# Kernel tuning notes

Measured on AMD Instinct MI355X. Metric: run time of the kernel, lower is better.

Reference implementation:

```python
import jax, jax.numpy as jnp
import numpy as np
from jax import lax

PS = 8  # patch size

def setup_inputs() -> dict:
    key = jax.random.key(0)
    ks = jax.random.split(key, 7)
    dim = 64
    B, H, W = 4, 256, 256
    x = jax.random.normal(ks[0], (B, dim, H, W), dtype=jnp.float32)
    # to_hidden: Conv2d(dim, 6*dim, k=1)
    w_hidden = jax.random.normal(ks[1], (6 * dim, dim, 1, 1), dtype=jnp.float32) * 0.05
    b_hidden = jax.random.normal(ks[2], (6 * dim,), dtype=jnp.float32) * 0.01
    # to_hidden_dw: depthwise Conv2d(6*dim, 6*dim, k=3, pad=1, groups=6*dim)
    w_dw = jax.random.normal(ks[3], (6 * dim, 1, 3, 3), dtype=jnp.float32) * 0.05
    b_dw = jax.random.normal(ks[4], (6 * dim,), dtype=jnp.float32) * 0.01
    # project_out: Conv2d(2*dim, dim, k=1)
    w_out = jax.random.normal(ks[5], (dim, 2 * dim, 1, 1), dtype=jnp.float32) * 0.05
    b_out = jax.random.normal(ks[6], (dim,), dtype=jnp.float32) * 0.01
    return {"x": x, "w_hidden": w_hidden, "b_hidden": b_hidden,
            "w_dw": w_dw, "b_dw": b_dw, "w_out": w_out, "b_out": b_out}

def _conv(x, w, groups=1, padding='VALID'):
    return lax.conv_general_dilated(
        x, w, window_strides=(1, 1), padding=padding,
        dimension_numbers=('NCHW', 'OIHW', 'NCHW'),
        feature_group_count=groups)

def reference(x, w_hidden, b_hidden, w_dw, b_dw, w_out, b_out):
    # 1x1 expansion to 6*dim channels
    hidden = _conv(x, w_hidden) + b_hidden[None, :, None, None]
    # 3x3 depthwise conv (groups == channels)
    dw = _conv(hidden, w_dw, groups=w_dw.shape[0], padding='SAME') + b_dw[None, :, None, None]
    q, k, v = jnp.split(dw, 3, axis=1)  # each (B, 2*dim, H, W)
    B, C, H, W = q.shape
    # raw reshape into (B,C,H/8,W/8,8,8) exactly as torch .reshape on contiguous NCHW
    q_patch = q.reshape(B, C, H // PS, W // PS, PS, PS)
    k_patch = k.reshape(B, C, H // PS, W // PS, PS, PS)
    q_fft = jnp.fft.rfft2(q_patch)
    k_fft = jnp.fft.rfft2(k_patch)
    out = jnp.fft.irfft2(q_fft * k_fft, s=(PS, PS))  # circular conv of q,k patches
    out = out.reshape(B, C, (H // PS) * PS, (W // PS) * PS)
    output = v * out
    output = _conv(output, w_out) + b_out[None, :, None, None]
    return output
```

## Files before the change

### kernel.cpp

```cpp
#include <hip/hip_runtime.h>

#define HW 65536
#define W_IMG 256
#define H_IMG 256
#define CIN 64
#define CHID 384
#define CQK 128

__global__ __launch_bounds__(256) void k1_expand(
    const float* __restrict__ x_base,
    const float* __restrict__ wh,
    const float* __restrict__ bh,
    float* __restrict__ hidden_base,
    size_t x_bstride, size_t hid_bstride)
{
    const float* x = x_base + blockIdx.z * x_bstride;
    float* hidden  = hidden_base + blockIdx.z * hid_bstride;
    const int pxbase = blockIdx.x * 256;
    const int cobase = blockIdx.y * 48;
    const int tid  = threadIdx.x;
    const int lane = tid & 63;
    const int wq   = __builtin_amdgcn_readfirstlane(tid >> 6);
    const int px   = pxbase + lane * 4;

    #pragma unroll
    for (int g = 0; g < 2; ++g) {
        const int cw = cobase + g * 24 + wq * 6;
        float acc[6][4];
        #pragma unroll
        for (int i = 0; i < 6; ++i)
            #pragma unroll
            for (int j = 0; j < 4; ++j) acc[i][j] = 0.f;

        float4 xa[4], xb[4];
        #pragma unroll
        for (int u = 0; u < 4; ++u)
            xa[u] = *reinterpret_cast<const float4*>(&x[(size_t)u * HW + px]);

        #pragma unroll 1
        for (int ci4 = 0; ci4 < CIN; ci4 += 8) {
            #pragma unroll
            for (int u = 0; u < 4; ++u)
                xb[u] = *reinterpret_cast<const float4*>(&x[(size_t)(ci4 + 4 + u) * HW + px]);
            #pragma unroll
            for (int i = 0; i < 6; ++i) {
                float4 wv = *reinterpret_cast<const float4*>(
                    &wh[(size_t)(cw + i) * CIN + ci4]);
                float wu[4] = {wv.x, wv.y, wv.z, wv.w};
                #pragma unroll
                for (int u = 0; u < 4; ++u) {
                    acc[i][0] += wu[u] * xa[u].x;
                    acc[i][1] += wu[u] * xa[u].y;
                    acc[i][2] += wu[u] * xa[u].z;
                    acc[i][3] += wu[u] * xa[u].w;
                }
            }
            if (ci4 + 8 < CIN) {
                #pragma unroll
                for (int u = 0; u < 4; ++u)
                    xa[u] = *reinterpret_cast<const float4*>(&x[(size_t)(ci4 + 8 + u) * HW + px]);
            }
            #pragma unroll
            for (int i = 0; i < 6; ++i) {
                float4 wv = *reinterpret_cast<const float4*>(
                    &wh[(size_t)(cw + i) * CIN + ci4 + 4]);
                float wu[4] = {wv.x, wv.y, wv.z, wv.w};
                #pragma unroll
                for (int u = 0; u < 4; ++u) {
                    acc[i][0] += wu[u] * xb[u].x;
                    acc[i][1] += wu[u] * xb[u].y;
                    acc[i][2] += wu[u] * xb[u].z;
                    acc[i][3] += wu[u] * xb[u].w;
                }
            }
        }

        #pragma unroll
        for (int i = 0; i < 6; ++i) {
            int co = cw + i;
            float b = bh[co];
            float4 o;
            o.x = acc[i][0] + b; o.y = acc[i][1] + b;
            o.z = acc[i][2] + b; o.w = acc[i][3] + b;
            *reinterpret_cast<float4*>(&hidden[(size_t)co * HW + px]) = o;
        }
    }
}

#define QK_CH   2208
#define QK_ROW  276
#define QK_SEG  68
__global__ __launch_bounds__(256) void k2_fused(
    const float* __restrict__ hidden_base,
    const float* __restrict__ wdw,
    const float* __restrict__ bdw,
    float* __restrict__ vout_base,
    size_t hid_bstride, size_t vout_bstride)
{
    __shared__ float qk[2 * QK_CH];

    const float* hidden = hidden_base + blockIdx.z * hid_bstride;
    float* vout         = vout_base + blockIdx.z * vout_bstride;

    const int c  = blockIdx.y;
    const int r0 = blockIdx.x * 8;
    const int tid = threadIdx.x;

    const int row   = tid >> 5;
    const int col32 = tid & 31;
    const int px8   = col32 * 8;
    const int gro   = r0 + row;

    float4 qa0[3], qa1[3], ka0[3], ka1[3];
    #pragma unroll
    for (int ky = 0; ky < 3; ++ky) {
        int grr = gro + ky - 1;
        qa0[ky] = make_float4(0.f,0.f,0.f,0.f); qa1[ky] = qa0[ky];
        ka0[ky] = qa0[ky];                      ka1[ky] = qa0[ky];
        if ((unsigned)grr < H_IMG) {
            const float* rq = hidden + (size_t)c * HW + (size_t)grr * W_IMG;
            const float* rk = hidden + (size_t)(c + CQK) * HW + (size_t)grr * W_IMG;
            qa0[ky] = *reinterpret_cast<const float4*>(&rq[px8]);
            qa1[ky] = *reinterpret_cast<const float4*>(&rq[px8 + 4]);
            ka0[ky] = *reinterpret_cast<const float4*>(&rk[px8]);
            ka1[ky] = *reinterpret_cast<const float4*>(&rk[px8 + 4]);
        }
    }

    #pragma unroll
    for (int ch = 0; ch < 2; ++ch) {
        const float4* a0 = ch ? ka0 : qa0;
        const float4* a1 = ch ? ka1 : qa1;
        const float* wv = wdw + (c + ch * CQK) * 9;
        const float bias = bdw[c + ch * CQK];

        float accd[8];
        #pragma unroll
        for (int j = 0; j < 8; ++j) accd[j] = bias;

        #pragma unroll
        for (int ky = 0; ky < 3; ++ky) {
            float kw0 = wv[ky * 3], kw1 = wv[ky * 3 + 1], kw2 = wv[ky * 3 + 2];
            float lf = __shfl_up(a1[ky].w, 1);
            float rt = __shfl_down(a0[ky].x, 1);
            if (col32 == 0)  lf = 0.f;
            if (col32 == 31) rt = 0.f;
            float h[10] = {lf, a0[ky].x, a0[ky].y, a0[ky].z, a0[ky].w,
                               a1[ky].x, a1[ky].y, a1[ky].z, a1[ky].w, rt};
            #pragma unroll
            for (int j = 0; j < 8; ++j)
                accd[j] += h[j] * kw0 + h[j + 1] * kw1 + h[j + 2] * kw2;
        }

        float* dst = &qk[ch * QK_CH + row * QK_ROW + (px8 >> 6) * QK_SEG + (px8 & 63)];
        float4 o0, o1;
        o0.x = accd[0]; o0.y = accd[1]; o0.z = accd[2]; o0.w = accd[3];
        o1.x = accd[4]; o1.y = accd[5]; o1.z = accd[6]; o1.w = accd[7];
        *reinterpret_cast<float4*>(dst)     = o0;
        *reinterpret_cast<float4*>(dst + 4) = o1;
    }

    const int seg = (tid >> 3) & 3;
    const int i   = tid & 7;
    const int gr  = r0 + row;
    const int wp0 = seg * 64 + i * 8;

    const float* hbv = hidden + (size_t)(c + 2 * CQK) * HW;
    float4 hv[3][2];
    float  hm[3], hp[3];
    #pragma unroll
    for (int ky = 0; ky < 3; ++ky) {
        int grr = gr + ky - 1;
        hv[ky][0] = make_float4(0.f,0.f,0.f,0.f);
        hv[ky][1] = make_float4(0.f,0.f,0.f,0.f);
        hm[ky] = 0.f; hp[ky] = 0.f;
        if ((unsigned)grr < H_IMG) {
            const float* rb = hbv + (size_t)grr * W_IMG;
            hv[ky][0] = *reinterpret_cast<const float4*>(&rb[wp0]);
            hv[ky][1] = *reinterpret_cast<const float4*>(&rb[wp0 + 4]);
            hm[ky] = (wp0 > 0)   ? rb[wp0 - 1] : 0.f;
            hp[ky] = (wp0 < 248) ? rb[wp0 + 8] : 0.f;
        }
    }

    __syncthreads();

    const float* qb = &qk[row * QK_ROW + seg * QK_SEG];
    const float* kb = &qk[QK_CH + row * QK_ROW + seg * QK_SEG];

    float acc[8];
    #pragma unroll
    for (int j = 0; j < 8; ++j) acc[j] = 0.f;

    #pragma unroll
    for (int s = 0; s < 8; ++s) {
        int qr = (i - s) & 7;
        float4 ka = *reinterpret_cast<const float4*>(&kb[s * 8]);
        float4 kc = *reinterpret_cast<const float4*>(&kb[s * 8 + 4]);
        float4 qa = *reinterpret_cast<const float4*>(&qb[qr * 8]);
        float4 qc = *reinterpret_cast<const float4*>(&qb[qr * 8 + 4]);
        float kr[8] = {ka.x, ka.y, ka.z, ka.w, kc.x, kc.y, kc.z, kc.w};
        float qv[8] = {qa.x, qa.y, qa.z, qa.w, qc.x, qc.y, qc.z, qc.w};
        #pragma unroll
        for (int t = 0; t < 8; ++t)
            #pragma unroll
            for (int j = 0; j < 8; ++j)
                acc[j] += kr[t] * qv[(j - t) & 7];
    }

    const float* wvv = wdw + (c + 2 * CQK) * 9;
    const float vbias = bdw[c + 2 * CQK];
    float vc[8];
    #pragma unroll
    for (int j = 0; j < 8; ++j) vc[j] = vbias;
    #pragma unroll
    for (int ky = 0; ky < 3; ++ky) {
        float kw0 = wvv[ky * 3], kw1 = wvv[ky * 3 + 1], kw2 = wvv[ky * 3 + 2];
        float h[10];
        h[0] = hm[ky];
        h[1] = hv[ky][0].x; h[2] = hv[ky][0].y; h[3] = hv[ky][0].z; h[4] = hv[ky][0].w;
        h[5] = hv[ky][1].x; h[6] = hv[ky][1].y; h[7] = hv[ky][1].z; h[8] = hv[ky][1].w;
        h[9] = hp[ky];
        #pragma unroll
        for (int j = 0; j < 8; ++j)
            vc[j] += h[j] * kw0 + h[j + 1] * kw1 + h[j + 2] * kw2;
    }

    float* dst = &vout[(size_t)c * HW + (size_t)gr * W_IMG + wp0];
    float4 o0, o1;
    o0.x = acc[0] * vc[0]; o0.y = acc[1] * vc[1];
    o0.z = acc[2] * vc[2]; o0.w = acc[3] * vc[3];
    o1.x = acc[4] * vc[4]; o1.y = acc[5] * vc[5];
    o1.z = acc[6] * vc[6]; o1.w = acc[7] * vc[7];
    *reinterpret_cast<float4*>(dst)     = o0;
    *reinterpret_cast<float4*>(dst + 4) = o1;
}

__global__ __launch_bounds__(256) void k3_project(
    const float* __restrict__ vout_base,
    const float* __restrict__ wo,
    const float* __restrict__ bo,
    float* __restrict__ out_base,
    size_t vout_bstride, size_t out_bstride)
{
    const float* vout = vout_base + blockIdx.z * vout_bstride;
    float* out        = out_base + blockIdx.z * out_bstride;
    const int pxbase = blockIdx.x * 256;
    const int cobase = blockIdx.y * 16;
    const int tid  = threadIdx.x;
    const int lane = tid & 63;
    const int wq   = __builtin_amdgcn_readfirstlane(tid >> 6);
    const int px   = pxbase + lane * 4;
    const int cw   = cobase + wq * 4;

    float acc[4][4];
    #pragma unroll
    for (int i = 0; i < 4; ++i)
        #pragma unroll
        for (int j = 0; j < 4; ++j) acc[i][j] = 0.f;

    float4 xa[4], xb[4];
    #pragma unroll
    for (int u = 0; u < 4; ++u)
        xa[u] = *reinterpret_cast<const float4*>(&vout[(size_t)u * HW + px]);

    #pragma unroll 1
    for (int cc4 = 0; cc4 < CQK; cc4 += 8) {
        #pragma unroll
        for (int u = 0; u < 4; ++u)
            xb[u] = *reinterpret_cast<const float4*>(&vout[(size_t)(cc4 + 4 + u) * HW + px]);
        #pragma unroll
        for (int i = 0; i < 4; ++i) {
            float4 wv = *reinterpret_cast<const float4*>(
                &wo[(size_t)(cw + i) * CQK + cc4]);
            float wu[4] = {wv.x, wv.y, wv.z, wv.w};
            #pragma unroll
            for (int u = 0; u < 4; ++u) {
                acc[i][0] += wu[u] * xa[u].x;
                acc[i][1] += wu[u] * xa[u].y;
                acc[i][2] += wu[u] * xa[u].z;
                acc[i][3] += wu[u] * xa[u].w;
            }
        }
        if (cc4 + 8 < CQK) {
            #pragma unroll
            for (int u = 0; u < 4; ++u)
                xa[u] = *reinterpret_cast<const float4*>(&vout[(size_t)(cc4 + 8 + u) * HW + px]);
        }
        #pragma unroll
        for (int i = 0; i < 4; ++i) {
            float4 wv = *reinterpret_cast<const float4*>(
                &wo[(size_t)(cw + i) * CQK + cc4 + 4]);
            float wu[4] = {wv.x, wv.y, wv.z, wv.w};
            #pragma unroll
            for (int u = 0; u < 4; ++u) {
                acc[i][0] += wu[u] * xb[u].x;
                acc[i][1] += wu[u] * xb[u].y;
                acc[i][2] += wu[u] * xb[u].z;
                acc[i][3] += wu[u] * xb[u].w;
            }
        }
    }

    #pragma unroll
    for (int i = 0; i < 4; ++i) {
        int co = cw + i;
        float b = bo[co];
        float4 o;
        o.x = acc[i][0] + b; o.y = acc[i][1] + b;
        o.z = acc[i][2] + b; o.w = acc[i][3] + b;
        *reinterpret_cast<float4*>(&out[(size_t)co * HW + px]) = o;
    }
}

extern "C" void kernel_launch(void* const* d_in, const int* in_sizes, int n_in,
                              void* d_out, int out_size, void* d_ws, size_t ws_size,
                              hipStream_t stream) {
    const float* x   = (const float*)d_in[0];
    const float* wh  = (const float*)d_in[1];
    const float* bh  = (const float*)d_in[2];
    const float* wdw = (const float*)d_in[3];
    const float* bdw = (const float*)d_in[4];
    const float* wo  = (const float*)d_in[5];
    const float* bo  = (const float*)d_in[6];
    float* out = (float*)d_out;

    const size_t n_hid  = (size_t)CHID * HW;
    const size_t n_vout = (size_t)CQK * HW;
    const size_t n_x    = (size_t)CIN * HW;

    if (ws_size >= 4 * (n_hid + n_vout) * sizeof(float)) {
        float* hidden = (float*)d_ws;
        float* vout   = hidden + 4 * n_hid;
        k1_expand <<<dim3(HW / 256, CHID / 48, 4), 256, 0, stream>>>(
            x, wh, bh, hidden, n_x, n_hid);
        k2_fused  <<<dim3(H_IMG / 8, CQK, 4),      256, 0, stream>>>(
            hidden, wdw, bdw, vout, n_hid, n_vout);
        k3_project<<<dim3(HW / 256, 64 / 16, 4),   256, 0, stream>>>(
            vout, wo, bo, out, n_vout, n_x);
    } else {
        float* hidden = (float*)d_ws;
        float* vout   = hidden + n_hid;
        for (int b = 0; b < 4; ++b) {
            const float* xb = x + (size_t)b * n_x;
            float* ob       = out + (size_t)b * n_x;
            k1_expand <<<dim3(HW / 256, CHID / 48, 1), 256, 0, stream>>>(
                xb, wh, bh, hidden, 0, 0);
            k2_fused  <<<dim3(H_IMG / 8, CQK, 1),      256, 0, stream>>>(
                hidden, wdw, bdw, vout, 0, 0);
            k3_project<<<dim3(HW / 256, 64 / 16, 1),   256, 0, stream>>>(
                vout, wo, bo, ob, 0, 0);
        }
    }
}
```

Before: 424.8 us.

## Widen k1 channel tile with triple-buffered loads; enlarge k2 row tile

After: 942.5 us. 122% more time.

```diff
diff --git a/kernel.cpp b/kernel.cpp
--- a/kernel.cpp
+++ b/kernel.cpp
@@ -6,6 +6,19 @@
 #define CIN 64
 #define CHID 384
 #define CQK 128
+
+#define K1_LOAD(B, CHUNK) { \
+    _Pragma("unroll") for (int u = 0; u < 4; ++u) \
+        B[u] = *reinterpret_cast<const float4*>(&x[(size_t)((CHUNK) * 4 + u) * HW + px]); }
+#define K1_COMP(B, CHUNK) { \
+    _Pragma("unroll") for (int i = 0; i < 12; ++i) { \
+        float4 wv = *reinterpret_cast<const float4*>(&wh[(size_t)(cw + i) * CIN + (CHUNK) * 4]); \
+        float wu[4] = {wv.x, wv.y, wv.z, wv.w}; \
+        _Pragma("unroll") for (int u = 0; u < 4; ++u) { \
+            acc[i][0] += wu[u] * B[u].x; \
+            acc[i][1] += wu[u] * B[u].y; \
+            acc[i][2] += wu[u] * B[u].z; \
+            acc[i][3] += wu[u] * B[u].w; } } }
 
 __global__ __launch_bounds__(256) void k1_expand(
     const float* __restrict__ x_base,
@@ -22,74 +35,75 @@
     const int lane = tid & 63;
     const int wq   = __builtin_amdgcn_readfirstlane(tid >> 6);
     const int px   = pxbase + lane * 4;
-
-    #pragma unroll
-    for (int g = 0; g < 2; ++g) {
-        const int cw = cobase + g * 24 + wq * 6;
-        float acc[6][4];
-        #pragma unroll
-        for (int i = 0; i < 6; ++i)
-            #pragma unroll
-            for (int j = 0; j < 4; ++j) acc[i][j] = 0.f;
-
-        float4 xa[4], xb[4];
-        #pragma unroll
-        for (int u = 0; u < 4; ++u)
-            xa[u] = *reinterpret_cast<const float4*>(&x[(size_t)u * HW + px]);
-
-        #pragma unroll 1
-        for (int ci4 = 0; ci4 < CIN; ci4 += 8) {
-            #pragma unroll
-            for (int u = 0; u < 4; ++u)
-                xb[u] = *reinterpret_cast<const float4*>(&x[(size_t)(ci4 + 4 + u) * HW + px]);
-            #pragma unroll
-            for (int i = 0; i < 6; ++i) {
-                float4 wv = *reinterpret_cast<const float4*>(
-                    &wh[(size_t)(cw + i) * CIN + ci4]);
-                float wu[4] = {wv.x, wv.y, wv.z, wv.w};
+    const int cw   = cobase + wq * 12;
+
+    float acc[12][4];
+    #pragma unroll
+    for (int i = 0; i < 12; ++i)
+        #pragma unroll
+        for (int j = 0; j < 4; ++j) acc[i][j] = 0.f;
+
+    float4 b0[4], b1[4], b2[4];
+    K1_LOAD(b0, 0)
+    K1_LOAD(b1, 1)
+
+    #pragma unroll
+    for (int t = 0; t < 16; ++t) {
+        if (t + 2 < 16) {
+            if (((t + 2) % 3) == 0)      { K1_LOAD(b0, t + 2) }
+            else if (((t + 2) % 3) == 1) { K1_LOAD(b1, t + 2) }
+            else                         { K1_LOAD(b2, t + 2) }
+        }
+        if ((t % 3) == 0)      { K1_COMP(b0, t) }
+        else if ((t % 3) == 1) { K1_COMP(b1, t) }
+        else                   { K1_COMP(b2, t) }
+    }
+
+    #pragma unroll
+    for (int i = 0; i < 12; ++i) {
+        int co = cw + i;
+        float b = bh[co];
+        float4 o;
+        o.x = acc[i][0] + b; o.y = acc[i][1] + b;
+        o.z = acc[i][2] + b; o.w = acc[i][3] + b;
+        *reinterpret_cast<float4*>(&hidden[(size_t)co * HW + px]) = o;
+    }
+}
+
+#define K2ROWS 32
+#define K2_CH  8704
+#define K2_ROW 272
+
+template<int I0>
+__device__ __forceinline__ void conv_half(
+    const float* __restrict__ qb, const float* __restrict__ kb, float acc[4][8])
+{
+    float qv[64];
+    #pragma unroll
+    for (int m = 0; m < 16; ++m) {
+        float4 t = *reinterpret_cast<const float4*>(&qb[m * 4]);
+        qv[m * 4]     = t.x;
+        qv[m * 4 + 1] = t.y;
+        qv[m * 4 + 2] = t.z;
+        qv[m * 4 + 3] = t.w;
+    }
+    #pragma unroll
+    for (int s = 0; s < 8; ++s) {
+        float4 ka = *reinterpret_cast<const float4*>(&kb[s * 8]);
+        float4 kc = *reinterpret_cast<const float4*>(&kb[s * 8 + 4]);
+        float kr[8] = {ka.x, ka.y, ka.z, ka.w, kc.x, kc.y, kc.z, kc.w};
+        #pragma unroll
+        for (int ii = 0; ii < 4; ++ii) {
+            const int qr = (I0 + ii - s) & 7;
+            #pragma unroll
+            for (int t = 0; t < 8; ++t)
                 #pragma unroll
-                for (int u = 0; u < 4; ++u) {
-                    acc[i][0] += wu[u] * xa[u].x;
-                    acc[i][1] += wu[u] * xa[u].y;
-                    acc[i][2] += wu[u] * xa[u].z;
-                    acc[i][3] += wu[u] * xa[u].w;
-                }
-            }
-            if (ci4 + 8 < CIN) {
-                #pragma unroll
-                for (int u = 0; u < 4; ++u)
-                    xa[u] = *reinterpret_cast<const float4*>(&x[(size_t)(ci4 + 8 + u) * HW + px]);
-            }
-            #pragma unroll
-            for (int i = 0; i < 6; ++i) {
-                float4 wv = *reinterpret_cast<const float4*>(
-                    &wh[(size_t)(cw + i) * CIN + ci4 + 4]);
-                float wu[4] = {wv.x, wv.y, wv.z, wv.w};
-                #pragma unroll
-                for (int u = 0; u < 4; ++u) {
-                    acc[i][0] += wu[u] * xb[u].x;
-                    acc[i][1] += wu[u] * xb[u].y;
-                    acc[i][2] += wu[u] * xb[u].z;
-                    acc[i][3] += wu[u] * xb[u].w;
-                }
-            }
-        }
-
-        #pragma unroll
-        for (int i = 0; i < 6; ++i) {
-            int co = cw + i;
-            float b = bh[co];
-            float4 o;
-            o.x = acc[i][0] + b; o.y = acc[i][1] + b;
-            o.z = acc[i][2] + b; o.w = acc[i][3] + b;
-            *reinterpret_cast<float4*>(&hidden[(size_t)co * HW + px]) = o;
-        }
-    }
-}
-
-#define QK_CH   2208
-#define QK_ROW  276
-#define QK_SEG  68
+                for (int j = 0; j < 8; ++j)
+                    acc[ii][j] += kr[t] * qv[qr * 8 + ((j - t) & 7)];
+        }
+    }
+}
+
 __global__ __launch_bounds__(256) void k2_fused(
     const float* __restrict__ hidden_base,
     const float* __restrict__ wdw,
@@ -97,143 +111,148 @@
     float* __restrict__ vout_base,
     size_t hid_bstride, size_t vout_bstride)
 {
-    __shared__ float qk[2 * QK_CH];
+    __shared__ float qk[2 * K2_CH];
 
     const float* hidden = hidden_base + blockIdx.z * hid_bstride;
     float* vout         = vout_base + blockIdx.z * vout_bstride;
 
     const int c  = blockIdx.y;
-    const int r0 = blockIdx.x * 8;
+    const int r0 = blockIdx.x * K2ROWS;
     const int tid = threadIdx.x;
 
-    const int row   = tid >> 5;
-    const int col32 = tid & 31;
-    const int px8   = col32 * 8;
-    const int gro   = r0 + row;
-
-    float4 qa0[3], qa1[3], ka0[3], ka1[3];
-    #pragma unroll
-    for (int ky = 0; ky < 3; ++ky) {
-        int grr = gro + ky - 1;
-        qa0[ky] = make_float4(0.f,0.f,0.f,0.f); qa1[ky] = qa0[ky];
-        ka0[ky] = qa0[ky];                      ka1[ky] = qa0[ky];
-        if ((unsigned)grr < H_IMG) {
-            const float* rq = hidden + (size_t)c * HW + (size_t)grr * W_IMG;
-            const float* rk = hidden + (size_t)(c + CQK) * HW + (size_t)grr * W_IMG;
-            qa0[ky] = *reinterpret_cast<const float4*>(&rq[px8]);
-            qa1[ky] = *reinterpret_cast<const float4*>(&rq[px8 + 4]);
-            ka0[ky] = *reinterpret_cast<const float4*>(&rk[px8]);
-            ka1[ky] = *reinterpret_cast<const float4*>(&rk[px8 + 4]);
-        }
-    }
-
-    #pragma unroll
-    for (int ch = 0; ch < 2; ++ch) {
-        const float4* a0 = ch ? ka0 : qa0;
-        const float4* a1 = ch ? ka1 : qa1;
-        const float* wv = wdw + (c + ch * CQK) * 9;
-        const float bias = bdw[c + ch * CQK];
-
-        float accd[8];
-        #pragma unroll
-        for (int j = 0; j < 8; ++j) accd[j] = bias;
-
-        #pragma unroll
-        for (int ky = 0; ky < 3; ++ky) {
-            float kw0 = wv[ky * 3], kw1 = wv[ky * 3 + 1], kw2 = wv[ky * 3 + 2];
-            float lf = __shfl_up(a1[ky].w, 1);
-            float rt = __shfl_down(a0[ky].x, 1);
-            if (col32 == 0)  lf = 0.f;
-            if (col32 == 31) rt = 0.f;
-            float h[10] = {lf, a0[ky].x, a0[ky].y, a0[ky].z, a0[ky].w,
-                               a1[ky].x, a1[ky].y, a1[ky].z, a1[ky].w, rt};
-            #pragma unroll
-            for (int j = 0; j < 8; ++j)
-                accd[j] += h[j] * kw0 + h[j + 1] * kw1 + h[j + 2] * kw2;
-        }
-
-        float* dst = &qk[ch * QK_CH + row * QK_ROW + (px8 >> 6) * QK_SEG + (px8 & 63)];
-        float4 o0, o1;
-        o0.x = accd[0]; o0.y = accd[1]; o0.z = accd[2]; o0.w = accd[3];
-        o1.x = accd[4]; o1.y = accd[5]; o1.z = accd[6]; o1.w = accd[7];
-        *reinterpret_cast<float4*>(dst)     = o0;
-        *reinterpret_cast<float4*>(dst + 4) = o1;
-    }
-
-    const int seg = (tid >> 3) & 3;
-    const int i   = tid & 7;
-    const int gr  = r0 + row;
-    const int wp0 = seg * 64 + i * 8;
-
-    const float* hbv = hidden + (size_t)(c + 2 * CQK) * HW;
-    float4 hv[3][2];
+    {
+        const int rowb  = tid >> 5;
+        const int col32 = tid & 31;
+        const int px8   = col32 * 8;
+        const float* wq9 = wdw + c * 9;
+        const float* wk9 = wdw + (c + CQK) * 9;
+        const float qb9 = bdw[c];
+        const float kb9 = bdw[c + CQK];
+
+        #pragma unroll
+        for (int rp = 0; rp < 4; ++rp) {
+            const int row_local = rp * 8 + rowb;
+            const int gro = r0 + row_local;
+
+            float4 qa0[3], qa1[3], ka0[3], ka1[3];
+            #pragma unroll
+            for (int ky = 0; ky < 3; ++ky) {
+                int grr = gro + ky - 1;
+                qa0[ky] = make_float4(0.f,0.f,0.f,0.f); qa1[ky] = qa0[ky];
+                ka0[ky] = qa0[ky];                      ka1[ky] = qa0[ky];
+                if ((unsigned)grr < H_IMG) {
+                    const float* rq = hidden + (size_t)c * HW + (size_t)grr * W_IMG;
+                    const float* rk = hidden + (size_t)(c + CQK) * HW + (size_t)grr * W_IMG;
+                    qa0[ky] = *reinterpret_cast<const float4*>(&rq[px8]);
+                    qa1[ky] = *reinterpret_cast<const float4*>(&rq[px8 + 4]);
+                    ka0[ky] = *reinterpret_cast<const float4*>(&rk[px8]);
+                    ka1[ky] = *reinterpret_cast<const float4*>(&rk[px8 + 4]);
+                }
+            }
+            #pragma unroll
+            for (int ch = 0; ch < 2; ++ch) {
+                const float4* a0 = ch ? ka0 : qa0;
+                const float4* a1 = ch ? ka1 : qa1;
+                const float* wv = ch ? wk9 : wq9;
+                float accd[8];
+                #pragma unroll
+                for (int j = 0; j < 8; ++j) accd[j] = ch ? kb9 : qb9;
+                #pragma unroll
+                for (int ky = 0; ky < 3; ++ky) {
+                    float kw0 = wv[ky * 3], kw1 = wv[ky * 3 + 1], kw2 = wv[ky * 3 + 2];
+                    float lf = __shfl_up(a1[ky].w, 1);
+                    float rt = __shfl_down(a0[ky].x, 1);
+                    if (col32 == 0)  lf = 0.f;
+                    if (col32 == 31) rt = 0.f;
+                    float h[10] = {lf, a0[ky].x, a0[ky].y, a0[ky].z, a0[ky].w,
+                                       a1[ky].x, a1[ky].y, a1[ky].z, a1[ky].w, rt};
+                    #pragma unroll
+                    for (int j = 0; j < 8; ++j)
+                        accd[j] += h[j] * kw0 + h[j + 1] * kw1 + h[j + 2] * kw2;
+                }
+                float* dst = &qk[ch * K2_CH + row_local * K2_ROW
+                                 + (px8 >> 6) * 68 + (px8 & 63)];
+                float4 o0, o1;
+                o0.x = accd[0]; o0.y = accd[1]; o0.z = accd[2]; o0.w = accd[3];
+                o1.x = accd[4]; o1.y = accd[5]; o1.z = accd[6]; o1.w = accd[7];
+                *reinterpret_cast<float4*>(dst)     = o0;
+                *reinterpret_cast<float4*>(dst + 4) = o1;
+            }
+        }
+    }
+
+    const int half = __builtin_amdgcn_readfirstlane(tid >> 7);
+    const int p    = tid & 127;
+    const int prow = p >> 2;
+    const int seg  = p & 3;
+    const int gr   = r0 + prow;
+    const int wp0  = seg * 64 + half * 32;
+
+    const float* rbv = hidden + (size_t)(c + 2 * CQK) * HW;
+    float4 hv[3][8];
     float  hm[3], hp[3];
     #pragma unroll
     for (int ky = 0; ky < 3; ++ky) {
         int grr = gr + ky - 1;
-        hv[ky][0] = make_float4(0.f,0.f,0.f,0.f);
-        hv[ky][1] = make_float4(0.f,0.f,0.f,0.f);
+        #pragma unroll
+        for (int u = 0; u < 8; ++u) hv[ky][u] = make_float4(0.f,0.f,0.f,0.f);
         hm[ky] = 0.f; hp[ky] = 0.f;
         if ((unsigned)grr < H_IMG) {
-            const float* rb = hbv + (size_t)grr * W_IMG;
-            hv[ky][0] = *reinterpret_cast<const float4*>(&rb[wp0]);
-            hv[ky][1] = *reinterpret_cast<const float4*>(&rb[wp0 + 4]);
-            hm[ky] = (wp0 > 0)   ? rb[wp0 - 1] : 0.f;
-            hp[ky] = (wp0 < 248) ? rb[wp0 + 8] : 0.f;
+            const float* rb = rbv + (size_t)grr * W_IMG;
+            #pragma unroll
+            for (int u = 0; u < 8; ++u)
+                hv[ky][u] = *reinterpret_cast<const float4*>(&rb[wp0 + u * 4]);
+            hm[ky] = (wp0 > 0)        ? rb[wp0 - 1]  : 0.f;
+            hp[ky] = (wp0 + 32 < 256) ? rb[wp0 + 32] : 0.f;
         }
     }
 
     __syncthreads();
-
-    const float* qb = &qk[row * QK_ROW + seg * QK_SEG];
-    const float* kb = &qk[QK_CH + row * QK_ROW + seg * QK_SEG];
-
-    float acc[8];
-    #pragma unroll
-    for (int j = 0; j < 8; ++j) acc[j] = 0.f;
-
-    #pragma unroll
-    for (int s = 0; s < 8; ++s) {
-        int qr = (i - s) & 7;
-        float4 ka = *reinterpret_cast<const float4*>(&kb[s * 8]);
-        float4 kc = *reinterpret_cast<const float4*>(&kb[s * 8 + 4]);
-        float4 qa = *reinterpret_cast<const float4*>(&qb[qr * 8]);
-        float4 qc = *reinterpret_cast<const float4*>(&qb[qr * 8 + 4]);
-        float kr[8] = {ka.x, ka.y, ka.z, ka.w, kc.x, kc.y, kc.z, kc.w};
-        float qv[8] = {qa.x, qa.y, qa.z, qa.w, qc.x, qc.y, qc.z, qc.w};
-        #pragma unroll
-        for (int t = 0; t < 8; ++t)
-            #pragma unroll
-            for (int j = 0; j < 8; ++j)
-                acc[j] += kr[t] * qv[(j - t) & 7];
-    }
 
     const float* wvv = wdw + (c + 2 * CQK) * 9;
     const float vbias = bdw[c + 2 * CQK];
-    float vc[8];
-    #pragma unroll
-    for (int j = 0; j < 8; ++j) vc[j] = vbias;
+    float vc[32];
+    #pragma unroll
+    for (int m = 0; m < 32; ++m) vc[m] = vbias;
     #pragma unroll
     for (int ky = 0; ky < 3; ++ky) {
         float kw0 = wvv[ky * 3], kw1 = wvv[ky * 3 + 1], kw2 = wvv[ky * 3 + 2];
-        float h[10];
+        float h[34];
         h[0] = hm[ky];
-        h[1] = hv[ky][0].x; h[2] = hv[ky][0].y; h[3] = hv[ky][0].z; h[4] = hv[ky][0].w;
-        h[5] = hv[ky][1].x; h[6] = hv[ky][1].y; h[7] = hv[ky][1].z; h[8] = hv[ky][1].w;
-        h[9] = hp[ky];
-        #pragma unroll
-        for (int j = 0; j < 8; ++j)
-            vc[j] += h[j] * kw0 + h[j + 1] * kw1 + h[j + 2] * kw2;
-    }
+        #pragma unroll
+        for (int u = 0; u < 8; ++u) {
+            h[1 + u * 4] = hv[ky][u].x; h[2 + u * 4] = hv[ky][u].y;
+            h[3 + u * 4] = hv[ky][u].z; h[4 + u * 4] = hv[ky][u].w;
+        }
+        h[33] = hp[ky];
+        #pragma unroll
+        for (int m = 0; m < 32; ++m)
+            vc[m] += h[m] * kw0 + h[m + 1] * kw1 + h[m + 2] * kw2;
+    }
+
+    const float* qb = &qk[prow * K2_ROW + seg * 68];
+    const float* kb = qb + K2_CH;
+
+    float acc[4][8];
+    #pragma unroll
+    for (int ii = 0; ii < 4; ++ii)
+        #pragma unroll
+        for (int j = 0; j < 8; ++j) acc[ii][j] = 0.f;
+
+    if (half == 0) conv_half<0>(qb, kb, acc);
+    else           conv_half<4>(qb, kb, acc);
 
     float* dst = &vout[(size_t)c * HW + (size_t)gr * W_IMG + wp0];
-    float4 o0, o1;
-    o0.x = acc[0] * vc[0]; o0.y = acc[1] * vc[1];
-    o0.z = acc[2] * vc[2]; o0.w = acc[3] * vc[3];
-    o1.x = acc[4] * vc[4]; o1.y = acc[5] * vc[5];
-    o1.z = acc[6] * vc[6]; o1.w = acc[7] * vc[7];
-    *reinterpret_cast<float4*>(dst)     = o0;
-    *reinterpret_cast<float4*>(dst + 4) = o1;
+    #pragma unroll
+    for (int ii = 0; ii < 4; ++ii) {
+        float4 o0, o1;
+        o0.x = acc[ii][0] * vc[ii * 8];     o0.y = acc[ii][1] * vc[ii * 8 + 1];
+        o0.z = acc[ii][2] * vc[ii * 8 + 2]; o0.w = acc[ii][3] * vc[ii * 8 + 3];
+        o1.x = acc[ii][4] * vc[ii * 8 + 4]; o1.y = acc[ii][5] * vc[ii * 8 + 5];
+        o1.z = acc[ii][6] * vc[ii * 8 + 6]; o1.w = acc[ii][7] * vc[ii * 8 + 7];
+        *reinterpret_cast<float4*>(dst + ii * 8)     = o0;
+        *reinterpret_cast<float4*>(dst + ii * 8 + 4) = o1;
+    }
 }
 
 __global__ __launch_bounds__(256) void k3_project(
@@ -332,11 +351,11 @@
     if (ws_size >= 4 * (n_hid + n_vout) * sizeof(float)) {
         float* hidden = (float*)d_ws;
         float* vout   = hidden + 4 * n_hid;
-        k1_expand <<<dim3(HW / 256, CHID / 48, 4), 256, 0, stream>>>(
+        k1_expand <<<dim3(HW / 256, CHID / 48, 4),    256, 0, stream>>>(
             x, wh, bh, hidden, n_x, n_hid);
-        k2_fused  <<<dim3(H_IMG / 8, CQK, 4),      256, 0, stream>>>(
+        k2_fused  <<<dim3(H_IMG / K2ROWS, CQK, 4),    256, 0, stream>>>(
             hidden, wdw, bdw, vout, n_hid, n_vout);
-        k3_project<<<dim3(HW / 256, 64 / 16, 4),   256, 0, stream>>>(
+        k3_project<<<dim3(HW / 256, 64 / 16, 4),      256, 0, stream>>>(
             vout, wo, bo, out, n_vout, n_x);
     } else {
         float* hidden = (float*)d_ws;
@@ -346,7 +365,7 @@
             float* ob       = out + (size_t)b * n_x;
             k1_expand <<<dim3(HW / 256, CHID / 48, 1), 256, 0, stream>>>(
                 xb, wh, bh, hidden, 0, 0);
-            k2_fused  <<<dim3(H_IMG / 8, CQK, 1),      256, 0, stream>>>(
+            k2_fused  <<<dim3(H_IMG / K2ROWS, CQK, 1), 256, 0, stream>>>(
                 hidden, wdw, bdw, vout, 0, 0);
             k3_project<<<dim3(HW / 256, 64 / 16, 1),   256, 0, stream>>>(
                 vout, wo, bo, ob, 0, 0);
```
